# Kernel optimization log

Measured on AMD Instinct MI355X. Metric: run time of the kernel, lower is better.

Reference implementation:

```python
import jax, jax.numpy as jnp
import numpy as np

SEQ = 2048
HID = 1024
NH = 16
HD = HID // NH


def setup_inputs() -> dict:
    key = jax.random.key(0)
    ks = jax.random.split(key, 5)
    s = 0.02
    return {
        "hidden_states": jax.random.normal(ks[0], (SEQ, HID), dtype=jnp.float32),
        "w_attn": jax.random.normal(ks[1], (HID, 3 * HID), dtype=jnp.float32) * s,
        "b_attn": jax.random.normal(ks[2], (3 * HID,), dtype=jnp.float32) * s,
        "w_proj": jax.random.normal(ks[3], (HID, HID), dtype=jnp.float32) * s,
        "b_proj": jax.random.normal(ks[4], (HID,), dtype=jnp.float32) * s,
    }


def reference(hidden_states, w_attn, b_attn, w_proj, b_proj):
    S = hidden_states.shape[0]
    qkv = hidden_states @ w_attn + b_attn          # [S, 3H]
    q, k, v = jnp.split(qkv, 3, axis=-1)
    q = q.reshape(S, NH, HD)
    k = k.reshape(S, NH, HD)
    v = v.reshape(S, NH, HD)
    sm_scale = 1.0 / np.sqrt(HD).astype(np.float32)
    # explicit scores [h, q, k] in fp32, as in the torch module
    scores = jnp.einsum('qhd,khd->hqk', q.astype(jnp.float32), k.astype(jnp.float32))
    scores = scores * sm_scale
    causal = jnp.tril(jnp.ones((S, S), dtype=bool))  # [q, k]
    scores = jnp.where(causal[None, :, :], scores, -jnp.inf)
    probs = jax.nn.softmax(scores, axis=-1)
    attn = jnp.einsum('hqk,khd->qhd', probs, v.astype(jnp.float32))  # [S, NH, HD]
    attn = attn.reshape(S, HID).astype(hidden_states.dtype)
    return attn @ w_proj + b_proj
```

## Files before the change

### kernel.cpp

```cpp
#include <hip/hip_runtime.h>
#include <cstdint>
#include <cstddef>

#define SEQ 2048
#define HID 1024
#define NHEAD 16
#define HDIM 64

typedef _Float16 f16;
typedef f16 half8 __attribute__((ext_vector_type(8)));
typedef f16 half4 __attribute__((ext_vector_type(4)));
typedef f16 half2_ __attribute__((ext_vector_type(2)));
typedef float f32x4 __attribute__((ext_vector_type(4)));

#define ASYNC_COPY16(g, l)                                                    \
  __builtin_amdgcn_global_load_lds(                                           \
      (const __attribute__((address_space(1))) void*)(const void*)(g),        \
      (__attribute__((address_space(3))) void*)(void*)(l), 16, 0, 0)

__global__ __launch_bounds__(256) void prologue(
    const float* __restrict__ h, const float* __restrict__ wa,
    const float* __restrict__ wp, f16* __restrict__ h16,
    f16* __restrict__ waT, f16* __restrict__ wpT) {
  const int b = blockIdx.x, tid = threadIdx.x;
  if (b >= 4096) {
    int i = ((b - 4096) * 256 + tid) * 4;
    float4 v = *(const float4*)(h + i);
    half4 o;
    o[0] = (f16)v.x; o[1] = (f16)v.y; o[2] = (f16)v.z; o[3] = (f16)v.w;
    *(half4*)(h16 + i) = o;
    return;
  }
  const float* src; f16* dst; int C, bx, by;
  if (b < 3072) { src = wa; dst = waT; C = 3072; bx = b % 96; by = b / 96; }
  else { int t = b - 3072; src = wp; dst = wpT; C = 1024; bx = t & 31; by = t >> 5; }
  __shared__ float tile[32][33];
  const int tx = tid & 31, ty = tid >> 5;
  const int c0 = bx * 32, r0 = by * 32;
#pragma unroll
  for (int i = 0; i < 32; i += 8)
    tile[ty + i][tx] = src[(size_t)(r0 + ty + i) * C + c0 + tx];
  __syncthreads();
#pragma unroll
  for (int i = 0; i < 32; i += 8)
    dst[(size_t)(c0 + ty + i) * 1024 + r0 + tx] = (f16)tile[tx][ty + i];
}

template <int BM, int BN, bool OUT16>
__global__ __launch_bounds__(256) void gemm_f16(
    const f16* __restrict__ A, const f16* __restrict__ Bt,
    const float* __restrict__ bias, void* __restrict__ Cout, int M, int N,
    int K) {
  constexpr int FM = BM / 32, FN = BN / 32;
  __shared__ __align__(16) f16 sA[BM * 32];
  __shared__ __align__(16) f16 sB[BN * 32];
  const int tid = threadIdx.x;
  const int wave = tid >> 6, lane = tid & 63;
  const int quad = lane >> 4, l16 = lane & 15;
  const int m0 = blockIdx.y * BM, n0 = blockIdx.x * BN;
  const int wm = (wave >> 1) * (BM / 2), wn = (wave & 1) * (BN / 2);
  const int rowA = lane >> 2, chunkA = lane & 3;

  f32x4 acc[FM][FN] = {};

  for (int k0 = 0; k0 < K; k0 += 32) {
#pragma unroll
    for (int r = wave; r < BM / 16; r += 4)
      ASYNC_COPY16(A + (size_t)(m0 + r * 16 + rowA) * K + k0 + chunkA * 8,
                   &sA[r * 512]);
#pragma unroll
    for (int r = wave; r < BN / 16; r += 4)
      ASYNC_COPY16(Bt + (size_t)(n0 + r * 16 + rowA) * K + k0 + chunkA * 8,
                   &sB[r * 512]);
    __syncthreads();

    half8 af[FM], bf[FN];
#pragma unroll
    for (int i = 0; i < FM; i++)
      af[i] = *(const half8*)&sA[(wm + i * 16 + l16) * 32 + quad * 8];
#pragma unroll
    for (int j = 0; j < FN; j++)
      bf[j] = *(const half8*)&sB[(wn + j * 16 + l16) * 32 + quad * 8];
#pragma unroll
    for (int i = 0; i < FM; i++)
#pragma unroll
      for (int j = 0; j < FN; j++)
        acc[i][j] = __builtin_amdgcn_mfma_f32_16x16x32_f16(af[i], bf[j],
                                                           acc[i][j], 0, 0, 0);
    __syncthreads();
  }

#pragma unroll
  for (int i = 0; i < FM; i++) {
    int row = m0 + wm + i * 16 + quad * 4;
#pragma unroll
    for (int j = 0; j < FN; j++) {
      int col = n0 + wn + j * 16 + l16;
      float bv = bias[col];
#pragma unroll
      for (int r = 0; r < 4; r++) {
        float v = acc[i][j][r] + bv;
        if (OUT16)
          ((f16*)Cout)[(size_t)(row + r) * N + col] = (f16)v;
        else
          ((float*)Cout)[(size_t)(row + r) * N + col] = v;
      }
    }
  }
}

#define LROW 72
__global__ __launch_bounds__(256, 3) void attn_split(
    const f16* __restrict__ qkv, f16* __restrict__ out,
    f16* __restrict__ Opart, float* __restrict__ ml) {
  const int b = blockIdx.x;
  const int h = b / 40;
  const int t = b % 40;
  int m, c, nc;
  if (t < 4)       { m = t;                 c = 0;      nc = 1; }
  else if (t < 12) { int u = t - 4;  m = 4 + (u >> 1);  c = u & 1; nc = 2; }
  else if (t < 24) { int u = t - 12; m = 8 + u / 3;     c = u % 3; nc = 3; }
  else             { int u = t - 24; m = 12 + (u >> 2); c = u & 3; nc = 4; }
  const int q0 = m * 128;
  const int T = 2 * m + 2;
  const int kt0 = c * 8;
  const int kt1 = (kt0 + 8 < T) ? kt0 + 8 : T;
  const int maskFrom = 2 * m;

  __shared__ __align__(16) f16 sK[64 * LROW];
  __shared__ __align__(16) f16 sVt[64 * LROW];
  __shared__ __align__(16) f16 sP[4][32 * LROW];

  const int tid = threadIdx.x;
  const int wave = tid >> 6, lane = tid & 63;
  const int quad = lane >> 4, l16 = lane & 15;

  const f16 qs = (f16)0.18033688f;
  half8 qf[2][2];
#pragma unroll
  for (int g = 0; g < 2; g++) {
    const f16* qb = qkv + (size_t)(q0 + wave * 32 + g * 16 + l16) * 3072 +
                    h * HDIM + quad * 8;
    qf[g][0] = *(const half8*)qb;
    qf[g][1] = *(const half8*)(qb + 32);
#pragma unroll
    for (int j = 0; j < 8; j++) { qf[g][0][j] *= qs; qf[g][1][j] *= qs; }
  }

  const f16* kbase = qkv + HID + h * HDIM;
  const f16* vbase = qkv + 2 * HID + h * HDIM;
  const int ks_row = tid >> 3, ks_cc = tid & 7;
  const int vs_d = tid & 63, vs_g = tid >> 6;

  f32x4 o[2][4] = {};
  float m_i[2] = {-1e30f, -1e30f}, l_i[2] = {0.f, 0.f};
  half8 kreg[2], vreg[2];

  auto prefetch = [&](int kt) {
    const int k0 = kt * 64;
#pragma unroll
    for (int i = 0; i < 2; i++) {
      kreg[i] = *(const half8*)(kbase + (size_t)(k0 + ks_row + i * 32) * 3072 +
                                ks_cc * 8);
      half8 col;
#pragma unroll
      for (int j = 0; j < 8; j++)
        col[j] = vbase[(size_t)(k0 + (vs_g + i * 4) * 8 + j) * 3072 + vs_d];
      vreg[i] = col;
    }
  };

  prefetch(kt0);
  for (int kt = kt0; kt < kt1; kt++) {
    const int k0 = kt * 64;
#pragma unroll
    for (int i = 0; i < 2; i++) {
      *(half8*)&sK[(ks_row + i * 32) * LROW + ks_cc * 8] = kreg[i];
      *(half8*)&sVt[vs_d * LROW + (vs_g + i * 4) * 8] = vreg[i];
    }
    __syncthreads();
    if (kt + 1 < kt1) prefetch(kt + 1);

    f32x4 sacc[2][4] = {};
#pragma unroll
    for (int kb = 0; kb < 4; kb++) {
      half8 kf0 = *(const half8*)&sK[(kb * 16 + l16) * LROW + quad * 8];
      half8 kf1 = *(const half8*)&sK[(kb * 16 + l16) * LROW + 32 + quad * 8];
#pragma unroll
      for (int g = 0; g < 2; g++) {
        sacc[g][kb] = __builtin_amdgcn_mfma_f32_16x16x32_f16(kf0, qf[g][0],
                                                             sacc[g][kb], 0, 0, 0);
        sacc[g][kb] = __builtin_amdgcn_mfma_f32_16x16x32_f16(kf1, qf[g][1],
                                                             sacc[g][kb], 0, 0, 0);
      }
    }
    if (kt >= maskFrom) {
#pragma unroll
      for (int g = 0; g < 2; g++) {
        const int qg = q0 + wave * 32 + g * 16 + l16;
#pragma unroll
        for (int kb = 0; kb < 4; kb++) {
          int kg = k0 + kb * 16 + quad * 4;
#pragma unroll
          for (int r = 0; r < 4; r++)
            if (kg + r > qg) sacc[g][kb][r] = -1e30f;
        }
      }
    }
#pragma unroll
    for (int g = 0; g < 2; g++) {
      float mx = -1e30f;
#pragma unroll
      for (int kb = 0; kb < 4; kb++)
#pragma unroll
        for (int r = 0; r < 4; r++) mx = fmaxf(mx, sacc[g][kb][r]);
      mx = fmaxf(mx, __shfl_xor(mx, 16));
      mx = fmaxf(mx, __shfl_xor(mx, 32));
      const float mnew = fmaxf(m_i[g], mx);
      const float alpha = exp2f(m_i[g] - mnew);
      float rs = 0.f;
#pragma unroll
      for (int kb = 0; kb < 4; kb++)
#pragma unroll
        for (int r = 0; r < 4; r++) {
          float p = exp2f(sacc[g][kb][r] - mnew);
          sacc[g][kb][r] = p;
          rs += p;
        }
      rs += __shfl_xor(rs, 16);
      rs += __shfl_xor(rs, 32);
      l_i[g] = l_i[g] * alpha + rs;
      m_i[g] = mnew;
#pragma unroll
      for (int j = 0; j < 4; j++)
#pragma unroll
        for (int r = 0; r < 4; r++) o[g][j][r] *= alpha;
      f16* pw = &sP[wave][(g * 16 + l16) * LROW];
#pragma unroll
      for (int kb = 0; kb < 4; kb++)
#pragma unroll
        for (int rp = 0; rp < 2; rp++) {
          half2_ pv;
          pv[0] = (f16)sacc[g][kb][rp * 2];
          pv[1] = (f16)sacc[g][kb][rp * 2 + 1];
          *(half2_*)&pw[kb * 16 + quad * 4 + rp * 2] = pv;
        }
    }
#pragma unroll
    for (int j = 0; j < 4; j++) {
      half8 vf0 = *(const half8*)&sVt[(j * 16 + l16) * LROW + quad * 8];
      half8 vf1 = *(const half8*)&sVt[(j * 16 + l16) * LROW + 32 + quad * 8];
#pragma unroll
      for (int g = 0; g < 2; g++) {
        half8 pf0 = *(const half8*)&sP[wave][(g * 16 + l16) * LROW + quad * 8];
        half8 pf1 =
            *(const half8*)&sP[wave][(g * 16 + l16) * LROW + 32 + quad * 8];
        o[g][j] = __builtin_amdgcn_mfma_f32_16x16x32_f16(vf0, pf0, o[g][j], 0, 0, 0);
        o[g][j] = __builtin_amdgcn_mfma_f32_16x16x32_f16(vf1, pf1, o[g][j], 0, 0, 0);
      }
    }
    __syncthreads();
  }

  if (nc == 1) {
#pragma unroll
    for (int g = 0; g < 2; g++) {
      const float inv = 1.f / l_i[g];
      f16* orow =
          out + (size_t)(q0 + wave * 32 + g * 16 + l16) * HID + h * HDIM;
#pragma unroll
      for (int j = 0; j < 4; j++) {
        half4 hv;
#pragma unroll
        for (int r = 0; r < 4; r++) hv[r] = (f16)(o[g][j][r] * inv);
        *(half4*)&orow[j * 16 + quad * 4] = hv;
      }
    }
  } else {
    int base;
    if (m < 8)       base = (m - 4) * 2;
    else if (m < 12) base = 8 + (m - 8) * 3;
    else             base = 20 + (m - 12) * 4;
    const int slot = h * 36 + base + c;
#pragma unroll
    for (int g = 0; g < 2; g++) {
      const int qrow = wave * 32 + g * 16 + l16;
      f16* op = Opart + (size_t)slot * 8192 + qrow * 64;
#pragma unroll
      for (int j = 0; j < 4; j++) {
        half4 hv;
#pragma unroll
        for (int r = 0; r < 4; r++) hv[r] = (f16)o[g][j][r];
        *(half4*)&op[j * 16 + quad * 4] = hv;
      }
      if (quad == 0) {
        ml[slot * 256 + qrow] = m_i[g];
        ml[slot * 256 + 128 + qrow] = l_i[g];
      }
    }
  }
}

__global__ __launch_bounds__(256) void attn_combine(
    const f16* __restrict__ Opart, const float* __restrict__ ml,
    f16* __restrict__ out) {
  int idx = blockIdx.x * 256 + threadIdx.x;
  int d = idx & 63;
  int row = (idx >> 6) & 127;
  int rest = idx >> 13;
  int mi = rest % 12;
  int h = rest / 12;
  int m = 4 + mi;
  int nc = (mi < 4) ? 2 : (mi < 8) ? 3 : 4;
  int base = (mi < 4) ? mi * 2 : (mi < 8) ? 8 + (mi - 4) * 3 : 20 + (mi - 8) * 4;
  int slot0 = h * 36 + base;

  float mm[4], ll[4];
  float M = -1e30f;
  for (int cc = 0; cc < nc; cc++) {
    mm[cc] = ml[(slot0 + cc) * 256 + row];
    ll[cc] = ml[(slot0 + cc) * 256 + 128 + row];
    M = fmaxf(M, mm[cc]);
  }
  float L = 0.f, acc = 0.f;
  for (int cc = 0; cc < nc; cc++) {
    float w = exp2f(mm[cc] - M);
    L += w * ll[cc];
    acc += w * (float)Opart[(size_t)(slot0 + cc) * 8192 + row * 64 + d];
  }
  out[(size_t)(m * 128 + row) * HID + h * HDIM + d] = (f16)(acc / L);
}

extern "C" void kernel_launch(void* const* d_in, const int* in_sizes, int n_in,
                              void* d_out, int out_size, void* d_ws,
                              size_t ws_size, hipStream_t stream) {
  const float* h = (const float*)d_in[0];
  const float* wa = (const float*)d_in[1];
  const float* ba = (const float*)d_in[2];
  const float* wp = (const float*)d_in[3];
  const float* bp = (const float*)d_in[4];
  float* out = (float*)d_out;

  char* ws = (char*)d_ws;
  f16* h16 = (f16*)(ws);
  f16* waT = (f16*)(ws + (4u << 20));
  f16* wpT = (f16*)(ws + (10u << 20));
  f16* qkv = (f16*)(ws + (12u << 20));
  f16* attn = (f16*)(ws + (24u << 20));
  f16* Opart = (f16*)(ws);
  float* mlbuf = (float*)(ws + 9437184);

  prologue<<<6144, 256, 0, stream>>>(h, wa, wp, h16, waT, wpT);
  gemm_f16<128, 128, true><<<dim3(24, 16), 256, 0, stream>>>(
      h16, waT, ba, qkv, SEQ, 3 * HID, HID);
  attn_split<<<640, 256, 0, stream>>>(qkv, attn, Opart, mlbuf);
  attn_combine<<<6144, 256, 0, stream>>>(Opart, mlbuf, attn);
  gemm_f16<64, 64, false><<<dim3(16, 32), 256, 0, stream>>>(
      attn, wpT, bp, out, SEQ, HID, HID);
}
```

Measured before the change: 160.5 us.

## Fuse hidden-state fp16 cast into QKV GEMM, finer attention splits, K-64 GEMM steps

Removes the separate fp32-to-fp16 cast of hidden_states and has the QKV GEMM read fp32 A directly and convert it while staging into LDS. The GEMM now consumes 64 K per barrier pair using two 32-wide LDS sub-tiles, and the QKV GEMM tile changes to 128x64. Attention is split into chunks of 4 key tiles instead of 8, giving 72 blocks per head and more combine work. P stores are widened to half4. The trade-off is more partial-output traffic and combine cost in exchange for better load balance, and synchronous fp32 A loads in place of async copies.

```diff
diff --git a/kernel.cpp b/kernel.cpp
--- a/kernel.cpp
+++ b/kernel.cpp
@@ -10,7 +10,6 @@
 typedef _Float16 f16;
 typedef f16 half8 __attribute__((ext_vector_type(8)));
 typedef f16 half4 __attribute__((ext_vector_type(4)));
-typedef f16 half2_ __attribute__((ext_vector_type(2)));
 typedef float f32x4 __attribute__((ext_vector_type(4)));
 
 #define ASYNC_COPY16(g, l)                                                    \
@@ -19,18 +18,9 @@
       (__attribute__((address_space(3))) void*)(void*)(l), 16, 0, 0)
 
 __global__ __launch_bounds__(256) void prologue(
-    const float* __restrict__ h, const float* __restrict__ wa,
-    const float* __restrict__ wp, f16* __restrict__ h16,
+    const float* __restrict__ wa, const float* __restrict__ wp,
     f16* __restrict__ waT, f16* __restrict__ wpT) {
   const int b = blockIdx.x, tid = threadIdx.x;
-  if (b >= 4096) {
-    int i = ((b - 4096) * 256 + tid) * 4;
-    float4 v = *(const float4*)(h + i);
-    half4 o;
-    o[0] = (f16)v.x; o[1] = (f16)v.y; o[2] = (f16)v.z; o[3] = (f16)v.w;
-    *(half4*)(h16 + i) = o;
-    return;
-  }
   const float* src; f16* dst; int C, bx, by;
   if (b < 3072) { src = wa; dst = waT; C = 3072; bx = b % 96; by = b / 96; }
   else { int t = b - 3072; src = wp; dst = wpT; C = 1024; bx = t & 31; by = t >> 5; }
@@ -46,14 +36,14 @@
     dst[(size_t)(c0 + ty + i) * 1024 + r0 + tx] = (f16)tile[tx][ty + i];
 }
 
-template <int BM, int BN, bool OUT16>
+template <int BM, int BN, bool OUT16, bool AF32>
 __global__ __launch_bounds__(256) void gemm_f16(
-    const f16* __restrict__ A, const f16* __restrict__ Bt,
+    const void* __restrict__ Ap, const f16* __restrict__ Bt,
     const float* __restrict__ bias, void* __restrict__ Cout, int M, int N,
     int K) {
   constexpr int FM = BM / 32, FN = BN / 32;
-  __shared__ __align__(16) f16 sA[BM * 32];
-  __shared__ __align__(16) f16 sB[BN * 32];
+  __shared__ __align__(16) f16 sA[2][BM * 32];
+  __shared__ __align__(16) f16 sB[2][BN * 32];
   const int tid = threadIdx.x;
   const int wave = tid >> 6, lane = tid & 63;
   const int quad = lane >> 4, l16 = lane & 15;
@@ -63,30 +53,58 @@
 
   f32x4 acc[FM][FN] = {};
 
-  for (int k0 = 0; k0 < K; k0 += 32) {
-#pragma unroll
-    for (int r = wave; r < BM / 16; r += 4)
-      ASYNC_COPY16(A + (size_t)(m0 + r * 16 + rowA) * K + k0 + chunkA * 8,
-                   &sA[r * 512]);
-#pragma unroll
-    for (int r = wave; r < BN / 16; r += 4)
-      ASYNC_COPY16(Bt + (size_t)(n0 + r * 16 + rowA) * K + k0 + chunkA * 8,
-                   &sB[r * 512]);
+  for (int k0 = 0; k0 < K; k0 += 64) {
+    if (AF32) {
+      const int row = tid >> 1, kh = (tid & 1) * 16;
+      const float* p0 = (const float*)Ap + (size_t)(m0 + row) * K + k0 + kh;
+#pragma unroll
+      for (int tt = 0; tt < 2; tt++) {
+        const float* p = p0 + tt * 32;
+        float4 a0 = ((const float4*)p)[0], a1 = ((const float4*)p)[1];
+        float4 a2 = ((const float4*)p)[2], a3 = ((const float4*)p)[3];
+        half8 h0, h1;
+        h0[0] = (f16)a0.x; h0[1] = (f16)a0.y; h0[2] = (f16)a0.z; h0[3] = (f16)a0.w;
+        h0[4] = (f16)a1.x; h0[5] = (f16)a1.y; h0[6] = (f16)a1.z; h0[7] = (f16)a1.w;
+        h1[0] = (f16)a2.x; h1[1] = (f16)a2.y; h1[2] = (f16)a2.z; h1[3] = (f16)a2.w;
+        h1[4] = (f16)a3.x; h1[5] = (f16)a3.y; h1[6] = (f16)a3.z; h1[7] = (f16)a3.w;
+        *(half8*)&sA[tt][row * 32 + kh] = h0;
+        *(half8*)&sA[tt][row * 32 + kh + 8] = h1;
+      }
+    } else {
+      const f16* A = (const f16*)Ap;
+#pragma unroll
+      for (int tt = 0; tt < 2; tt++)
+#pragma unroll
+        for (int r = wave; r < BM / 16; r += 4)
+          ASYNC_COPY16(
+              A + (size_t)(m0 + r * 16 + rowA) * K + k0 + tt * 32 + chunkA * 8,
+              &sA[tt][r * 512]);
+    }
+#pragma unroll
+    for (int tt = 0; tt < 2; tt++)
+#pragma unroll
+      for (int r = wave; r < BN / 16; r += 4)
+        ASYNC_COPY16(
+            Bt + (size_t)(n0 + r * 16 + rowA) * K + k0 + tt * 32 + chunkA * 8,
+            &sB[tt][r * 512]);
     __syncthreads();
 
-    half8 af[FM], bf[FN];
-#pragma unroll
-    for (int i = 0; i < FM; i++)
-      af[i] = *(const half8*)&sA[(wm + i * 16 + l16) * 32 + quad * 8];
-#pragma unroll
-    for (int j = 0; j < FN; j++)
-      bf[j] = *(const half8*)&sB[(wn + j * 16 + l16) * 32 + quad * 8];
-#pragma unroll
-    for (int i = 0; i < FM; i++)
+#pragma unroll
+    for (int tt = 0; tt < 2; tt++) {
+      half8 af[FM], bf[FN];
+#pragma unroll
+      for (int i = 0; i < FM; i++)
+        af[i] = *(const half8*)&sA[tt][(wm + i * 16 + l16) * 32 + quad * 8];
 #pragma unroll
       for (int j = 0; j < FN; j++)
-        acc[i][j] = __builtin_amdgcn_mfma_f32_16x16x32_f16(af[i], bf[j],
-                                                           acc[i][j], 0, 0, 0);
+        bf[j] = *(const half8*)&sB[tt][(wn + j * 16 + l16) * 32 + quad * 8];
+#pragma unroll
+      for (int i = 0; i < FM; i++)
+#pragma unroll
+        for (int j = 0; j < FN; j++)
+          acc[i][j] = __builtin_amdgcn_mfma_f32_16x16x32_f16(af[i], bf[j],
+                                                             acc[i][j], 0, 0, 0);
+    }
     __syncthreads();
   }
 
@@ -114,17 +132,23 @@
     const f16* __restrict__ qkv, f16* __restrict__ out,
     f16* __restrict__ Opart, float* __restrict__ ml) {
   const int b = blockIdx.x;
-  const int h = b / 40;
-  const int t = b % 40;
-  int m, c, nc;
-  if (t < 4)       { m = t;                 c = 0;      nc = 1; }
-  else if (t < 12) { int u = t - 4;  m = 4 + (u >> 1);  c = u & 1; nc = 2; }
-  else if (t < 24) { int u = t - 12; m = 8 + u / 3;     c = u % 3; nc = 3; }
-  else             { int u = t - 24; m = 12 + (u >> 2); c = u & 3; nc = 4; }
+  const int h = b / 72;
+  const int t = b % 72;
+  int m, c, nc, base = 0;
+  if (t < 2) { m = t; c = 0; nc = 1; }
+  else {
+    int s = t - 2, acc = 0;
+    m = 2; c = 0; nc = 2;
+    for (int mm = 2; mm <= 15; mm++) {
+      int n = (2 * mm + 5) >> 2;
+      if (s < acc + n) { m = mm; c = s - acc; nc = n; base = acc; break; }
+      acc += n;
+    }
+  }
   const int q0 = m * 128;
   const int T = 2 * m + 2;
-  const int kt0 = c * 8;
-  const int kt1 = (kt0 + 8 < T) ? kt0 + 8 : T;
+  const int kt0 = c * 4;
+  const int kt1 = (kt0 + 4 < T) ? kt0 + 4 : T;
   const int maskFrom = 2 * m;
 
   __shared__ __align__(16) f16 sK[64 * LROW];
@@ -237,14 +261,12 @@
         for (int r = 0; r < 4; r++) o[g][j][r] *= alpha;
       f16* pw = &sP[wave][(g * 16 + l16) * LROW];
 #pragma unroll
-      for (int kb = 0; kb < 4; kb++)
-#pragma unroll
-        for (int rp = 0; rp < 2; rp++) {
-          half2_ pv;
-          pv[0] = (f16)sacc[g][kb][rp * 2];
-          pv[1] = (f16)sacc[g][kb][rp * 2 + 1];
-          *(half2_*)&pw[kb * 16 + quad * 4 + rp * 2] = pv;
-        }
+      for (int kb = 0; kb < 4; kb++) {
+        half4 pv;
+#pragma unroll
+        for (int r = 0; r < 4; r++) pv[r] = (f16)sacc[g][kb][r];
+        *(half4*)&pw[kb * 16 + quad * 4] = pv;
+      }
     }
 #pragma unroll
     for (int j = 0; j < 4; j++) {
@@ -277,11 +299,7 @@
       }
     }
   } else {
-    int base;
-    if (m < 8)       base = (m - 4) * 2;
-    else if (m < 12) base = 8 + (m - 8) * 3;
-    else             base = 20 + (m - 12) * 4;
-    const int slot = h * 36 + base + c;
+    const int slot = h * 70 + base + c;
 #pragma unroll
     for (int g = 0; g < 2; g++) {
       const int qrow = wave * 32 + g * 16 + l16;
@@ -308,24 +326,21 @@
   int d = idx & 63;
   int row = (idx >> 6) & 127;
   int rest = idx >> 13;
-  int mi = rest % 12;
-  int h = rest / 12;
-  int m = 4 + mi;
-  int nc = (mi < 4) ? 2 : (mi < 8) ? 3 : 4;
-  int base = (mi < 4) ? mi * 2 : (mi < 8) ? 8 + (mi - 4) * 3 : 20 + (mi - 8) * 4;
-  int slot0 = h * 36 + base;
-
-  float mm[4], ll[4];
+  int mi = rest % 14;
+  int h = rest / 14;
+  int m = 2 + mi;
+  int nc = (2 * m + 5) >> 2;
+  int base = 0;
+  for (int j = 2; j < m; j++) base += (2 * j + 5) >> 2;
+  int slot0 = h * 70 + base;
+
   float M = -1e30f;
-  for (int cc = 0; cc < nc; cc++) {
-    mm[cc] = ml[(slot0 + cc) * 256 + row];
-    ll[cc] = ml[(slot0 + cc) * 256 + 128 + row];
-    M = fmaxf(M, mm[cc]);
-  }
+  for (int cc = 0; cc < nc; cc++)
+    M = fmaxf(M, ml[(slot0 + cc) * 256 + row]);
   float L = 0.f, acc = 0.f;
   for (int cc = 0; cc < nc; cc++) {
-    float w = exp2f(mm[cc] - M);
-    L += w * ll[cc];
+    float w = exp2f(ml[(slot0 + cc) * 256 + row] - M);
+    L += w * ml[(slot0 + cc) * 256 + 128 + row];
     acc += w * (float)Opart[(size_t)(slot0 + cc) * 8192 + row * 64 + d];
   }
   out[(size_t)(m * 128 + row) * HID + h * HDIM + d] = (f16)(acc / L);
@@ -342,19 +357,18 @@
   float* out = (float*)d_out;
 
   char* ws = (char*)d_ws;
-  f16* h16 = (f16*)(ws);
-  f16* waT = (f16*)(ws + (4u << 20));
-  f16* wpT = (f16*)(ws + (10u << 20));
-  f16* qkv = (f16*)(ws + (12u << 20));
-  f16* attn = (f16*)(ws + (24u << 20));
-  f16* Opart = (f16*)(ws);
-  float* mlbuf = (float*)(ws + 9437184);
-
-  prologue<<<6144, 256, 0, stream>>>(h, wa, wp, h16, waT, wpT);
-  gemm_f16<128, 128, true><<<dim3(24, 16), 256, 0, stream>>>(
-      h16, waT, ba, qkv, SEQ, 3 * HID, HID);
-  attn_split<<<640, 256, 0, stream>>>(qkv, attn, Opart, mlbuf);
-  attn_combine<<<6144, 256, 0, stream>>>(Opart, mlbuf, attn);
-  gemm_f16<64, 64, false><<<dim3(16, 32), 256, 0, stream>>>(
+  f16* waT = (f16*)(ws);
+  f16* wpT = (f16*)(ws + (6u << 20));
+  f16* qkv = (f16*)(ws + (8u << 20));
+  f16* attn = (f16*)(ws + (20u << 20));
+  f16* Opart = (f16*)(ws + (24u << 20));
+  float* mlbuf = (float*)(ws + (24u << 20) + 18350080);
+
+  prologue<<<4096, 256, 0, stream>>>(wa, wp, waT, wpT);
+  gemm_f16<128, 64, true, true><<<dim3(48, 16), 256, 0, stream>>>(
+      h, waT, ba, qkv, SEQ, 3 * HID, HID);
+  attn_split<<<1152, 256, 0, stream>>>(qkv, attn, Opart, mlbuf);
+  attn_combine<<<7168, 256, 0, stream>>>(Opart, mlbuf, attn);
+  gemm_f16<64, 64, false, false><<<dim3(16, 32), 256, 0, stream>>>(
       attn, wpT, bp, out, SEQ, HID, HID);
 }
```

Measured after the change: 176.3 us. +9.8%, slower.
